# Kernel optimization log

Measured on AMD Instinct MI355X. Metric: run time of the kernel, lower is better.

Reference implementation:

```python
import jax, jax.numpy as jnp
import numpy as np

B, C, Lc, Vc = 16, 8, 30, 10000
Lp, Vp = 64, 2000
N_IV = 128
BETA_C = 0.7
BETA_P = 0.7


def setup_inputs() -> dict:
    key = jax.random.key(0)
    ks = jax.random.split(key, 9)
    pred_captions = jax.random.normal(ks[0], (B, C, Lc, Vc), jnp.float32)
    gt_captions = jax.random.randint(ks[1], (B, C, Lc), 0, Vc)
    gt_cap_lens = jax.random.randint(ks[2], (B, C), 1, Lc + 1).astype(jnp.int32)
    gt_caps_count = jax.random.randint(ks[3], (B,), 1, C + 1).astype(jnp.int32)
    pred_program = jax.random.normal(ks[4], (B, Lp, Vp), jnp.float32)
    gt_program = jax.random.randint(ks[5], (B, Lp), 0, Vp)
    gt_prog_len = jax.random.randint(ks[6], (B,), 1, Lp + 1).astype(jnp.int32)
    # intervals [N,2,1]: sort along dim 1 so end >= start (well-conditioned union)
    pred_intervals = jnp.sort(jax.random.uniform(ks[7], (N_IV, 2, 1), jnp.float32), axis=1)
    gt_intervals = jnp.sort(jax.random.uniform(ks[8], (N_IV, 2, 1), jnp.float32), axis=1)
    scores = jnp.ones((3,), jnp.float32)  # config.combination_scores
    return dict(gt_captions=gt_captions, gt_cap_lens=gt_cap_lens,
                pred_captions=pred_captions, gt_program=gt_program,
                gt_prog_len=gt_prog_len, pred_program=pred_program,
                gt_intervals=gt_intervals, pred_intervals=pred_intervals,
                gt_caps_count=gt_caps_count, scores=scores)


def _sentlen_loss(logits, targets, lens, item_mask, beta):
    """SentenceLengthLoss ('mean'): -sum_t logsoftmax[t, tgt_t] / len_i**beta, / n_items.
    logits [..., T, V]; targets [..., T] int; lens [...] int; item_mask [...] bool.
    Masked form is exactly equivalent to the torch ragged gather/concat packing.
    """
    T = logits.shape[-2]
    tok_mask = (jnp.arange(T) < lens[..., None]) & item_mask[..., None]  # [..., T]
    logp = jax.nn.log_softmax(logits, axis=-1)
    tok_lp = jnp.take_along_axis(logp, targets[..., None], axis=-1)[..., 0]  # [..., T]
    w = jnp.where(item_mask,
                  1.0 / jnp.maximum(lens, 1).astype(jnp.float32) ** beta,
                  0.0)  # per-sentence weight 1/len**beta
    loss_sum = -jnp.sum(w[..., None] * jnp.where(tok_mask, tok_lp, 0.0))
    n_items = jnp.sum(item_mask.astype(jnp.float32))
    return loss_sum / n_items


def _iou_loss(pred_iv, gt_iv):
    # pred_iv, gt_iv: [N, 2, 1] (start, end)
    p0, p1 = pred_iv[:, 0, 0], pred_iv[:, 1, 0]
    g0, g1 = gt_iv[:, 0, 0], gt_iv[:, 1, 0]
    inter = jnp.clip(jnp.minimum(p1, g1) - jnp.maximum(p0, g0), 0.0)
    union = jnp.maximum(p1, g1) - jnp.minimum(p0, g0)
    return 1.0 - jnp.sum(inter / union) / pred_iv.shape[0]


def reference(gt_captions, gt_cap_lens, pred_captions, gt_program, gt_prog_len,
              pred_program, gt_intervals, pred_intervals, gt_caps_count, scores):
    # captions: caption i of video j is active iff i < gt_caps_count[j]
    cap_item_mask = jnp.arange(pred_captions.shape[1])[None, :] < gt_caps_count[:, None]
    cap_loss = _sentlen_loss(pred_captions, gt_captions, gt_cap_lens,
                             cap_item_mask, BETA_C)
    # program: one sequence per batch element, all active
    prog_item_mask = jnp.ones((pred_program.shape[0],), bool)
    prog_loss = _sentlen_loss(pred_program, gt_program, gt_prog_len,
                              prog_item_mask, BETA_P)
    iou_loss = _iou_loss(pred_intervals, gt_intervals)
    losses = jnp.stack([cap_loss, prog_loss, iou_loss])
    loss = jnp.sum(scores * losses)
    return (loss, cap_loss, prog_loss, iou_loss)
```

## Files before the change

### kernel.cpp

```cpp
#include <hip/hip_runtime.h>
#include <math.h>

#define B   16
#define C   8
#define LC  30
#define VC  10000
#define LP  64
#define VP  2000
#define N_IV 128
#define BETA 0.7f

constexpr int CAP_ROWS  = B * C * LC;
constexpr int PROG_ROWS = B * LP;

__global__ __launch_bounds__(256) void rows_kernel(
    const float* __restrict__ pred_cap,  const int* __restrict__ gt_cap,
    const int*  __restrict__ cap_lens,   const int* __restrict__ caps_count,
    const float* __restrict__ pred_prog, const int* __restrict__ gt_prog,
    const int*  __restrict__ prog_len,
    float* __restrict__ cap_part, float* __restrict__ prog_part)
{
    const int bid = blockIdx.x;
    const int tid = threadIdx.x;

    const float* row;
    float*       outp;
    int          tgt, V;
    float        w;

    if (bid < CAP_ROWS) {
        const int b   = bid / (C * LC);
        const int rem = bid % (C * LC);
        const int c   = rem / LC;
        const int t   = rem % LC;
        const int cnt = caps_count[b];
        const int len = cap_lens[b * C + c];
        if (c >= cnt || t >= len) {
            if (tid == 0) cap_part[bid] = 0.0f;
            return;
        }
        row  = pred_cap + (size_t)bid * VC;
        tgt  = gt_cap[bid];
        w    = powf((float)len, -BETA);
        outp = cap_part + bid;
        V    = VC;
    } else {
        const int pbid = bid - CAP_ROWS;
        const int b    = pbid / LP;
        const int t    = pbid % LP;
        const int len  = prog_len[b];
        if (t >= len) {
            if (tid == 0) prog_part[pbid] = 0.0f;
            return;
        }
        row  = pred_prog + (size_t)pbid * VP;
        tgt  = gt_prog[pbid];
        w    = powf((float)len, -BETA);
        outp = prog_part + pbid;
        V    = VP;
    }

    float m = -INFINITY, s = 0.0f;
    const float4* row4 = (const float4*)row;
    const int n4 = V >> 2;
    for (int j = tid; j < n4; j += 256) {
        float4 v = row4[j];
        float mx = fmaxf(fmaxf(v.x, v.y), fmaxf(v.z, v.w));
        float mn = fmaxf(m, mx);
        s = s * __expf(m - mn)
          + __expf(v.x - mn) + __expf(v.y - mn)
          + __expf(v.z - mn) + __expf(v.w - mn);
        m = mn;
    }

    #pragma unroll
    for (int off = 1; off < 64; off <<= 1) {
        float m2 = __shfl_xor(m, off, 64);
        float s2 = __shfl_xor(s, off, 64);
        float mn = fmaxf(m, m2);
        s = s * __expf(m - mn) + s2 * __expf(m2 - mn);
        m = mn;
    }

    __shared__ float sm[4], ss[4];
    const int wid = tid >> 6;
    if ((tid & 63) == 0) { sm[wid] = m; ss[wid] = s; }
    __syncthreads();

    if (tid == 0) {
        float M = sm[0], S = ss[0];
        #pragma unroll
        for (int i = 1; i < 4; i++) {
            float mn = fmaxf(M, sm[i]);
            S = S * __expf(M - mn) + ss[i] * __expf(sm[i] - mn);
            M = mn;
        }
        const float lse    = M + logf(S);
        const float logp_t = row[tgt] - lse;
        *outp = -w * logp_t;
    }
}

__device__ inline float wave_sum(float v) {
    #pragma unroll
    for (int off = 32; off; off >>= 1) v += __shfl_xor(v, off, 64);
    return v;
}

__global__ __launch_bounds__(256) void finish_kernel(
    const float* __restrict__ cap_part, const float* __restrict__ prog_part,
    const int*  __restrict__ caps_count,
    const float* __restrict__ pred_iv, const float* __restrict__ gt_iv,
    const float* __restrict__ scores, float* __restrict__ out)
{
    const int tid = threadIdx.x;

    float cs = 0.0f;
    for (int i = tid; i < CAP_ROWS; i += 256) cs += cap_part[i];
    float ps = 0.0f;
    for (int i = tid; i < PROG_ROWS; i += 256) ps += prog_part[i];

    float is = 0.0f;
    if (tid < N_IV) {
        const float p0 = pred_iv[tid * 2 + 0];
        const float p1 = pred_iv[tid * 2 + 1];
        const float g0 = gt_iv[tid * 2 + 0];
        const float g1 = gt_iv[tid * 2 + 1];
        const float inter = fmaxf(fminf(p1, g1) - fmaxf(p0, g0), 0.0f);
        const float uni   = fmaxf(p1, g1) - fminf(p0, g0);
        is = inter / uni;
    }

    float nc = 0.0f;
    if (tid < B) nc = (float)caps_count[tid];

    cs = wave_sum(cs);
    ps = wave_sum(ps);
    is = wave_sum(is);
    nc = wave_sum(nc);

    __shared__ float red[4][4];
    const int wid = tid >> 6;
    if ((tid & 63) == 0) {
        red[0][wid] = cs; red[1][wid] = ps; red[2][wid] = is; red[3][wid] = nc;
    }
    __syncthreads();

    if (tid == 0) {
        float CS = red[0][0] + red[0][1] + red[0][2] + red[0][3];
        float PS = red[1][0] + red[1][1] + red[1][2] + red[1][3];
        float IS = red[2][0] + red[2][1] + red[2][2] + red[2][3];
        float NC = red[3][0] + red[3][1] + red[3][2] + red[3][3];

        const float cap_loss  = CS / NC;
        const float prog_loss = PS / (float)B;
        const float iou_loss  = 1.0f - IS / (float)N_IV;
        const float loss = scores[0] * cap_loss + scores[1] * prog_loss
                         + scores[2] * iou_loss;
        out[0] = loss;
        out[1] = cap_loss;
        out[2] = prog_loss;
        out[3] = iou_loss;
    }
}

extern "C" void kernel_launch(void* const* d_in, const int* in_sizes, int n_in,
                              void* d_out, int out_size, void* d_ws, size_t ws_size,
                              hipStream_t stream) {
    const int*   gt_captions    = (const int*)  d_in[0];
    const int*   gt_cap_lens    = (const int*)  d_in[1];
    const float* pred_captions  = (const float*)d_in[2];
    const int*   gt_program     = (const int*)  d_in[3];
    const int*   gt_prog_len    = (const int*)  d_in[4];
    const float* pred_program   = (const float*)d_in[5];
    const float* gt_intervals   = (const float*)d_in[6];
    const float* pred_intervals = (const float*)d_in[7];
    const int*   gt_caps_count  = (const int*)  d_in[8];
    const float* scores         = (const float*)d_in[9];
    float* out = (float*)d_out;

    float* cap_part  = (float*)d_ws;
    float* prog_part = cap_part + CAP_ROWS;

    rows_kernel<<<CAP_ROWS + PROG_ROWS, 256, 0, stream>>>(
        pred_captions, gt_captions, gt_cap_lens, gt_caps_count,
        pred_program, gt_program, gt_prog_len,
        cap_part, prog_part);

    finish_kernel<<<1, 256, 0, stream>>>(
        cap_part, prog_part, gt_caps_count,
        pred_intervals, gt_intervals, scores, out);
}
```

Baseline: 23.76 us.

## Register-cache softmax rows with two-pass max/sum and wave-per-row program rows

Each caption row is loaded once into registers as float4 values, then reduced in two passes (block max, then exp-sum) instead of an online rescaling softmax. This removes the per-element rescale exponentials. Program rows are now handled one per wavefront, four per block, which cuts the program block count by four. The cost is more registers per thread and an extra block barrier for the max.

```diff
diff --git a/kernel.cpp b/kernel.cpp
--- a/kernel.cpp
+++ b/kernel.cpp
@@ -10,8 +10,13 @@
 #define N_IV 128
 #define BETA 0.7f
 
-constexpr int CAP_ROWS  = B * C * LC;
-constexpr int PROG_ROWS = B * LP;
+constexpr int CAP_ROWS    = B * C * LC;
+constexpr int PROG_ROWS   = B * LP;
+constexpr int PROG_BLOCKS = PROG_ROWS / 4;
+constexpr int N4C = VC / 4;
+constexpr int KC  = (N4C + 255) / 256;
+constexpr int N4P = VP / 4;
+constexpr int KP  = (N4P + 63) / 64;
 
 __global__ __launch_bounds__(256) void rows_kernel(
     const float* __restrict__ pred_cap,  const int* __restrict__ gt_cap,
@@ -20,84 +25,105 @@
     const int*  __restrict__ prog_len,
     float* __restrict__ cap_part, float* __restrict__ prog_part)
 {
+    __shared__ float sred[4];
+    __shared__ float ssum[4];
+
     const int bid = blockIdx.x;
     const int tid = threadIdx.x;
-
-    const float* row;
-    float*       outp;
-    int          tgt, V;
-    float        w;
 
     if (bid < CAP_ROWS) {
         const int b   = bid / (C * LC);
         const int rem = bid % (C * LC);
         const int c   = rem / LC;
         const int t   = rem % LC;
-        const int cnt = caps_count[b];
         const int len = cap_lens[b * C + c];
-        if (c >= cnt || t >= len) {
+        if (c >= caps_count[b] || t >= len) {
             if (tid == 0) cap_part[bid] = 0.0f;
             return;
         }
-        row  = pred_cap + (size_t)bid * VC;
-        tgt  = gt_cap[bid];
-        w    = powf((float)len, -BETA);
-        outp = cap_part + bid;
-        V    = VC;
+        const float*  row  = pred_cap + (size_t)bid * VC;
+        const float4* row4 = (const float4*)row;
+
+        float4 v[KC];
+        #pragma unroll
+        for (int k = 0; k < KC; k++) {
+            const int j = tid + k * 256;
+            if (j < N4C) v[k] = row4[j];
+            else v[k] = make_float4(-INFINITY, -INFINITY, -INFINITY, -INFINITY);
+        }
+
+        float m = -INFINITY;
+        #pragma unroll
+        for (int k = 0; k < KC; k++)
+            m = fmaxf(m, fmaxf(fmaxf(v[k].x, v[k].y), fmaxf(v[k].z, v[k].w)));
+        #pragma unroll
+        for (int off = 32; off; off >>= 1) m = fmaxf(m, __shfl_xor(m, off, 64));
+
+        const int wid = tid >> 6;
+        if ((tid & 63) == 0) sred[wid] = m;
+        __syncthreads();
+        const float M = fmaxf(fmaxf(sred[0], sred[1]), fmaxf(sred[2], sred[3]));
+
+        float s = 0.0f;
+        #pragma unroll
+        for (int k = 0; k < KC; k++)
+            s += __expf(v[k].x - M) + __expf(v[k].y - M)
+               + __expf(v[k].z - M) + __expf(v[k].w - M);
+        #pragma unroll
+        for (int off = 32; off; off >>= 1) s += __shfl_xor(s, off, 64);
+
+        if ((tid & 63) == 0) ssum[wid] = s;
+        __syncthreads();
+
+        if (tid == 0) {
+            const float S   = ssum[0] + ssum[1] + ssum[2] + ssum[3];
+            const float lse = M + logf(S);
+            const float w   = powf((float)len, -BETA);
+            cap_part[bid] = -w * (row[gt_cap[bid]] - lse);
+        }
     } else {
-        const int pbid = bid - CAP_ROWS;
-        const int b    = pbid / LP;
-        const int t    = pbid % LP;
+        const int pb   = bid - CAP_ROWS;
+        const int lane = tid & 63;
+        const int wid  = tid >> 6;
+        const int r    = pb * 4 + wid;
+        const int b    = r / LP;
+        const int t    = r % LP;
         const int len  = prog_len[b];
         if (t >= len) {
-            if (tid == 0) prog_part[pbid] = 0.0f;
+            if (lane == 0) prog_part[r] = 0.0f;
             return;
         }
-        row  = pred_prog + (size_t)pbid * VP;
-        tgt  = gt_prog[pbid];
-        w    = powf((float)len, -BETA);
-        outp = prog_part + pbid;
-        V    = VP;
-    }
-
-    float m = -INFINITY, s = 0.0f;
-    const float4* row4 = (const float4*)row;
-    const int n4 = V >> 2;
-    for (int j = tid; j < n4; j += 256) {
-        float4 v = row4[j];
-        float mx = fmaxf(fmaxf(v.x, v.y), fmaxf(v.z, v.w));
-        float mn = fmaxf(m, mx);
-        s = s * __expf(m - mn)
-          + __expf(v.x - mn) + __expf(v.y - mn)
-          + __expf(v.z - mn) + __expf(v.w - mn);
-        m = mn;
-    }
-
-    #pragma unroll
-    for (int off = 1; off < 64; off <<= 1) {
-        float m2 = __shfl_xor(m, off, 64);
-        float s2 = __shfl_xor(s, off, 64);
-        float mn = fmaxf(m, m2);
-        s = s * __expf(m - mn) + s2 * __expf(m2 - mn);
-        m = mn;
-    }
-
-    __shared__ float sm[4], ss[4];
-    const int wid = tid >> 6;
-    if ((tid & 63) == 0) { sm[wid] = m; ss[wid] = s; }
-    __syncthreads();
-
-    if (tid == 0) {
-        float M = sm[0], S = ss[0];
-        #pragma unroll
-        for (int i = 1; i < 4; i++) {
-            float mn = fmaxf(M, sm[i]);
-            S = S * __expf(M - mn) + ss[i] * __expf(sm[i] - mn);
-            M = mn;
-        }
-        const float lse    = M + logf(S);
-        const float logp_t = row[tgt] - lse;
-        *outp = -w * logp_t;
+        const float*  row  = pred_prog + (size_t)r * VP;
+        const float4* row4 = (const float4*)row;
+
+        float4 v[KP];
+        #pragma unroll
+        for (int k = 0; k < KP; k++) {
+            const int j = lane + k * 64;
+            if (j < N4P) v[k] = row4[j];
+            else v[k] = make_float4(-INFINITY, -INFINITY, -INFINITY, -INFINITY);
+        }
+
+        float m = -INFINITY;
+        #pragma unroll
+        for (int k = 0; k < KP; k++)
+            m = fmaxf(m, fmaxf(fmaxf(v[k].x, v[k].y), fmaxf(v[k].z, v[k].w)));
+        #pragma unroll
+        for (int off = 32; off; off >>= 1) m = fmaxf(m, __shfl_xor(m, off, 64));
+
+        float s = 0.0f;
+        #pragma unroll
+        for (int k = 0; k < KP; k++)
+            s += __expf(v[k].x - m) + __expf(v[k].y - m)
+               + __expf(v[k].z - m) + __expf(v[k].w - m);
+        #pragma unroll
+        for (int off = 32; off; off >>= 1) s += __shfl_xor(s, off, 64);
+
+        if (lane == 0) {
+            const float lse = m + logf(s);
+            const float w   = powf((float)len, -BETA);
+            prog_part[r] = -w * (row[gt_prog[r]] - lse);
+        }
     }
 }
 
@@ -147,10 +173,10 @@
     __syncthreads();
 
     if (tid == 0) {
-        float CS = red[0][0] + red[0][1] + red[0][2] + red[0][3];
-        float PS = red[1][0] + red[1][1] + red[1][2] + red[1][3];
-        float IS = red[2][0] + red[2][1] + red[2][2] + red[2][3];
-        float NC = red[3][0] + red[3][1] + red[3][2] + red[3][3];
+        const float CS = red[0][0] + red[0][1] + red[0][2] + red[0][3];
+        const float PS = red[1][0] + red[1][1] + red[1][2] + red[1][3];
+        const float IS = red[2][0] + red[2][1] + red[2][2] + red[2][3];
+        const float NC = red[3][0] + red[3][1] + red[3][2] + red[3][3];
 
         const float cap_loss  = CS / NC;
         const float prog_loss = PS / (float)B;
@@ -182,7 +208,7 @@
     float* cap_part  = (float*)d_ws;
     float* prog_part = cap_part + CAP_ROWS;
 
-    rows_kernel<<<CAP_ROWS + PROG_ROWS, 256, 0, stream>>>(
+    rows_kernel<<<CAP_ROWS + PROG_BLOCKS, 256, 0, stream>>>(
         pred_captions, gt_captions, gt_cap_lens, gt_caps_count,
         pred_program, gt_program, gt_prog_len,
         cap_part, prog_part);
```

Result: faster. 22.77 us (-4.2%).
